# Kernel optimization log

Hardware: AMD Instinct MI355X
Metric: run time of the kernel (lower is better)

The kernel has to match this reference:

```python
import jax, jax.numpy as jnp
import numpy as np

NUM_HEADS = 12


def setup_inputs() -> dict:
    key = jax.random.key(0)
    ks = jax.random.split(key, 6)
    B, H, W, C = 8, 32, 32, 768
    hd = C // NUM_HEADS
    n = lambda k, shp, sc: jax.random.normal(k, shp, dtype=jnp.float32) * sc
    return {
        "x": n(ks[0], (B, H, W, C), 1.0),
        "qkv_w": n(ks[1], (3 * C, C), 0.02),
        "qkv_b": jnp.zeros((3 * C,), jnp.float32),
        "proj_w": n(ks[2], (C, C), 0.02),
        "proj_b": jnp.zeros((C,), jnp.float32),
        "rel_pos_h": n(ks[3], (2 * H - 1, hd), 0.02),
        "rel_pos_w": n(ks[4], (2 * W - 1, hd), 0.02),
    }


def reference(x, qkv_w, qkv_b, proj_w, proj_b, rel_pos_h, rel_pos_w):
    B, H, W, C = x.shape
    nH = NUM_HEADS
    hd = C // nH
    scale = hd ** -0.5
    # qkv projection (torch Linear convention: y = x @ W.T + b)
    qkv = x.reshape(B, H * W, C) @ qkv_w.T + qkv_b              # (B, HW, 3C)
    qkv = qkv.reshape(B, H * W, 3, nH, hd).transpose(2, 0, 3, 1, 4)
    qkv = qkv.reshape(3, B * nH, H * W, hd)
    q, k, v = qkv[0], qkv[1], qkv[2]
    attn = jnp.einsum('bqd,bkd->bqk', q * scale, k)             # (B*nH, HW, HW)
    # decomposed relative position bias (q_size == k_size, so no interpolation)
    coords_h = jnp.arange(H)[:, None] - jnp.arange(H)[None, :] + (H - 1)
    coords_w = jnp.arange(W)[:, None] - jnp.arange(W)[None, :] + (W - 1)
    Rh = rel_pos_h[coords_h]                                    # (H, H, hd)
    Rw = rel_pos_w[coords_w]                                    # (W, W, hd)
    r_q = q.reshape(B * nH, H, W, hd)
    rel_h = jnp.einsum('bhwc,hkc->bhwk', r_q, Rh)               # (B*nH, H, W, H)
    rel_w = jnp.einsum('bhwc,wkc->bhwk', r_q, Rw)               # (B*nH, H, W, W)
    attn = (attn.reshape(B * nH, H, W, H, W)
            + rel_h[..., :, None] + rel_w[..., None, :]).reshape(B * nH, H * W, H * W)
    attn = jax.nn.softmax(attn, axis=-1)
    out = attn @ v                                              # (B*nH, HW, hd)
    out = out.reshape(B, nH, H, W, hd).transpose(0, 2, 3, 1, 4).reshape(B, H, W, C)
    return out @ proj_w.T + proj_b
```

## Files before the change

kernel.cpp:

```cpp
#include <hip/hip_runtime.h>

using u16 = unsigned short;
using u32 = unsigned int;
typedef __attribute__((ext_vector_type(8))) short bf16x8;
typedef __attribute__((ext_vector_type(4))) float f32x4;

__device__ __forceinline__ float bf2f(u32 h) {
  union { u32 u; float f; } c; c.u = h << 16; return c.f;
}
__device__ __forceinline__ u16 f2bf(float f) {
  union { float f; u32 u; } c; c.f = f;
  u32 u = c.u;
  u32 r = (u + 0x7FFFu + ((u >> 16) & 1u)) >> 16;
  return (u16)r;
}

#define GLD16(gsrc, ldst)                                                      \
  __builtin_amdgcn_global_load_lds(                                            \
      (const __attribute__((address_space(1))) unsigned int*)(gsrc),           \
      (__attribute__((address_space(3))) unsigned int*)(ldst), 16, 0, 0)

__device__ __forceinline__ int kappa(int ss) {
  return (ss & 0x23) | ((ss & 0x10) >> 2) | ((ss & 0x0C) << 1);
}

__global__ void cvt_kernel(const float* __restrict__ src, u16* __restrict__ dst, int n) {
  int i = (blockIdx.x * blockDim.x + threadIdx.x) * 4;
  if (i < n) {
    float4 v = *(const float4*)(src + i);
    ushort4 o;
    o.x = f2bf(v.x); o.y = f2bf(v.y); o.z = f2bf(v.z); o.w = f2bf(v.w);
    *(ushort4*)(dst + i) = o;
  }
}

__global__ void tbl_kernel(const float* __restrict__ rph, const float* __restrict__ rpw,
                           u16* __restrict__ tbl) {
  int i = blockIdx.x * 256 + threadIdx.x;
  int row = i >> 6, d = i & 63;
  float v = 0.f;
  if (row < 63) v = rph[row * 64 + d];
  else if (row >= 64 && row < 127) v = rpw[(row - 64) * 64 + d];
  tbl[i] = f2bf(v * 8.0f);
}

__global__ void aug_kernel(u16* __restrict__ kb) {
  int j = blockIdx.x * 256 + threadIdx.x;
  int g = j >> 4, q4 = j & 15;
  int s = g & 1023;
  int d0 = 64 + q4 * 4;
  int kwslot = 64 + (s & 31);
  int khslot = 96 + (s >> 5);
  ushort4 v;
  v.x = (d0 == kwslot || d0 == khslot) ? 0x3F80 : 0;
  v.y = (d0 + 1 == kwslot || d0 + 1 == khslot) ? 0x3F80 : 0;
  v.z = (d0 + 2 == kwslot || d0 + 2 == khslot) ? 0x3F80 : 0;
  v.w = (d0 + 3 == kwslot || d0 + 3 == khslot) ? 0x3F80 : 0;
  *(ushort4*)&kb[(size_t)g * 128 + d0] = v;
}

__global__ __launch_bounds__(256, 2) void pgemm_kernel(
    const u16* __restrict__ A, const u16* __restrict__ tbl, u16* __restrict__ Q2) {
  __shared__ u16 As[128 * 64];
  __shared__ u16 Bs[128 * 64];
  const int tid = threadIdx.x;
  const int lane = tid & 63, wave = tid >> 6;
  const int lr = lane & 15, lg = lane >> 4;
  const int m0 = blockIdx.x * 128;
  const int wm = (wave >> 1) * 64, wn = (wave & 1) * 64;

#pragma unroll
  for (int i = 0; i < 4; ++i) {
    int c = tid + i * 256;
    int row = c >> 3, pp = c & 7;
    int pl = pp ^ (row & 7);
    GLD16(A + (size_t)(m0 + row) * 128 + pl * 8, &As[c * 8]);
    GLD16(tbl + row * 64 + pl * 8, &Bs[c * 8]);
  }
  __syncthreads();

  bf16x8 a[4][2], b[4][2];
#pragma unroll
  for (int m = 0; m < 4; ++m) {
    int row = wm + m * 16 + lr;
#pragma unroll
    for (int kf = 0; kf < 2; ++kf)
      a[m][kf] = *(const bf16x8*)&As[(row * 64 + kf * 32 + lg * 8) ^ ((row & 7) << 3)];
  }
#pragma unroll
  for (int n = 0; n < 4; ++n) {
    int row = wn + n * 16 + lr;
#pragma unroll
    for (int kf = 0; kf < 2; ++kf)
      b[n][kf] = *(const bf16x8*)&Bs[(row * 64 + kf * 32 + lg * 8) ^ ((row & 7) << 3)];
  }

  f32x4 acc[4][4] = {};
#pragma unroll
  for (int kf = 0; kf < 2; ++kf)
#pragma unroll
    for (int m = 0; m < 4; ++m)
#pragma unroll
      for (int n = 0; n < 4; ++n)
        acc[m][n] = __builtin_amdgcn_mfma_f32_16x16x32_bf16(a[m][kf], b[n][kf], acc[m][n], 0, 0, 0);

#pragma unroll
  for (int m = 0; m < 4; ++m)
#pragma unroll
    for (int n = 0; n < 4; ++n) {
      const int col = wn + n * 16 + lr;
#pragma unroll
      for (int r = 0; r < 4; ++r) {
        const int g = m0 + wm + m * 16 + lg * 4 + r;
        const int s = g & 1023;
        const int hq = s >> 5, w = s & 31;
        u16 hv = f2bf(acc[m][n][r]);
        if (col < 64) {
          int kh = hq + 31 - col;
          if ((unsigned)kh < 32u) Q2[(size_t)g * 128 + 96 + kh] = hv;
        } else {
          int kw = w + 95 - col;
          if ((unsigned)kw < 32u) Q2[(size_t)g * 128 + 64 + kw] = hv;
        }
      }
    }
}

template <int MODE>
__global__ __launch_bounds__(512, 2) void gemm128(
    const u16* __restrict__ A, const u16* __restrict__ B,
    const float* __restrict__ bias, u16* __restrict__ oq, u16* __restrict__ ok,
    u16* __restrict__ ovt, float* __restrict__ ofp) {
  __shared__ u16 As[2][128 * 64];
  __shared__ u16 Bs[2][128 * 64];
  const int tid = threadIdx.x;
  const int lane = tid & 63, wave = tid >> 6;
  const int lr = lane & 15, lg = lane >> 4;

  const int nbx = (MODE == 0) ? 18 : 6;
  const int nwg = nbx * 64;
  int id = blockIdx.y * nbx + blockIdx.x;
  int nid = (id & 7) * (nwg >> 3) + (id >> 3);
  const int m0 = (nid / nbx) * 128, n0 = (nid % nbx) * 128;
  const int wm = (wave >> 2) * 64, wn = (wave & 3) * 32;

  f32x4 acc[4][2] = {};

  const u16* ap[2];
  const u16* bp[2];
#pragma unroll
  for (int i = 0; i < 2; ++i) {
    int c = tid + i * 512;
    int row = c >> 3, pp = c & 7;
    int pl = pp ^ (row & 7);
    if constexpr (MODE == 0) {
      ap[i] = A + (size_t)(m0 + row) * 768 + pl * 8;
    } else {
      int g = m0 + row;
      ap[i] = A + ((size_t)((g >> 10) * 12) << 16) + (g & 1023) * 64 + pl * 8;
    }
    bp[i] = B + (size_t)(n0 + row) * 768 + pl * 8;
  }
  constexpr int dA = (MODE == 0) ? 64 : 65536;

  auto stage = [&](int bi) {
#pragma unroll
    for (int i = 0; i < 2; ++i) {
      int c = tid + i * 512;
      GLD16(ap[i], &As[bi][c * 8]);
      GLD16(bp[i], &Bs[bi][c * 8]);
      ap[i] += dA;
      bp[i] += 64;
    }
  };

  stage(0);
#pragma unroll 1
  for (int t = 0; t < 12; ++t) {
    const int cur = t & 1;
    if (t < 11) {
      stage(cur ^ 1);
      asm volatile("s_waitcnt vmcnt(4)" ::: "memory");
    } else {
      asm volatile("s_waitcnt vmcnt(0)" ::: "memory");
    }
    __builtin_amdgcn_sched_barrier(0);
    __builtin_amdgcn_s_barrier();
    __builtin_amdgcn_sched_barrier(0);

    bf16x8 a[4][2], b[2][2];
#pragma unroll
    for (int m = 0; m < 4; ++m) {
      int row = wm + m * 16 + lr;
#pragma unroll
      for (int kf = 0; kf < 2; ++kf)
        a[m][kf] = *(const bf16x8*)&As[cur][(row * 64 + kf * 32 + lg * 8) ^ ((row & 7) << 3)];
    }
#pragma unroll
    for (int n = 0; n < 2; ++n) {
      int row = wn + n * 16 + lr;
#pragma unroll
      for (int kf = 0; kf < 2; ++kf)
        b[n][kf] = *(const bf16x8*)&Bs[cur][(row * 64 + kf * 32 + lg * 8) ^ ((row & 7) << 3)];
    }
    __builtin_amdgcn_s_setprio(1);
#pragma unroll
    for (int kf = 0; kf < 2; ++kf)
#pragma unroll
      for (int m = 0; m < 4; ++m)
#pragma unroll
        for (int n = 0; n < 2; ++n)
          acc[m][n] = __builtin_amdgcn_mfma_f32_16x16x32_bf16(a[m][kf], b[n][kf], acc[m][n], 0, 0, 0);
    __builtin_amdgcn_s_setprio(0);

    __builtin_amdgcn_sched_barrier(0);
    __builtin_amdgcn_s_barrier();
    __builtin_amdgcn_sched_barrier(0);
  }

#pragma unroll
  for (int m = 0; m < 4; ++m) {
    const int grow0 = m0 + wm + m * 16 + lg * 4;
#pragma unroll
    for (int n = 0; n < 2; ++n) {
      const int gcol = n0 + wn + n * 16 + lr;
      const float bv = bias[gcol];
      if constexpr (MODE == 0) {
        int which = (gcol >= 1536) ? 2 : (gcol >= 768 ? 1 : 0);
        int rem = gcol - which * 768;
        int bh = (grow0 >> 10) * 12 + (rem >> 6);
        if (which == 2) {
          int s0 = grow0 & 1023;
          int colb = (s0 & ~63) | kappa(s0 & 63);
          ushort4 pk;
          pk.x = f2bf(acc[m][n][0] + bv);
          pk.y = f2bf(acc[m][n][1] + bv);
          pk.z = f2bf(acc[m][n][2] + bv);
          pk.w = f2bf(acc[m][n][3] + bv);
          *(ushort4*)&ovt[((size_t)bh << 16) + (size_t)(rem & 63) * 1024 + colb] = pk;
        } else {
          u16* dst = (which == 0) ? oq : ok;
          const float sc = (which == 0) ? 0.18033688f : 1.0f;
#pragma unroll
          for (int r = 0; r < 4; ++r) {
            int s = (grow0 & 1023) + r;
            dst[((size_t)bh << 17) + s * 128 + (rem & 63)] = f2bf((acc[m][n][r] + bv) * sc);
          }
        }
      } else {
#pragma unroll
        for (int r = 0; r < 4; ++r)
          ofp[(size_t)(grow0 + r) * 768 + gcol] = acc[m][n][r] + bv;
      }
    }
  }
}

__global__ __launch_bounds__(256, 2) void attn_kernel(
    const u16* __restrict__ qb, const u16* __restrict__ kb,
    const u16* __restrict__ vtb, u16* __restrict__ ao) {
  __shared__ u16 Ks[2][8192];
  __shared__ u16 Vs[2][4096];

  const int tid = threadIdx.x;
  const int lane = tid & 63, wave = tid >> 6;
  const int lr = lane & 15, lg = lane >> 4;
  const int bh = blockIdx.x;
  const int q0 = blockIdx.y * 128 + wave * 32;
  const size_t hb2 = (size_t)bh << 17;
  const size_t hbv = (size_t)bh << 16;

  bf16x8 qf[2][4];
#pragma unroll
  for (int m = 0; m < 2; ++m)
#pragma unroll
    for (int kf = 0; kf < 4; ++kf)
      qf[m][kf] = *(const bf16x8*)(qb + hb2 + (size_t)(q0 + m * 16 + lr) * 128 + kf * 32 + lg * 8);

  float lsum[2] = {};
  f32x4 acco[2][4] = {};

  const u16* kp[4];
  const u16* vp[2];
#pragma unroll
  for (int i = 0; i < 4; ++i) {
    int c = tid + i * 256;
    int half = c >> 9, row = (c >> 3) & 63, pp = c & 7;
    int pl = pp ^ (row & 7);
    kp[i] = kb + hb2 + (size_t)row * 128 + half * 64 + pl * 8;
  }
#pragma unroll
  for (int i = 0; i < 2; ++i) {
    int c = tid + i * 256;
    int row = c >> 3, pp = c & 7;
    int pl = pp ^ (row & 7);
    vp[i] = vtb + hbv + (size_t)row * 1024 + pl * 8;
  }

  auto stage = [&](int bi) {
#pragma unroll
    for (int i = 0; i < 4; ++i) {
      int c = tid + i * 256;
      GLD16(kp[i], &Ks[bi][c * 8]);
      kp[i] += 8192;
    }
#pragma unroll
    for (int i = 0; i < 2; ++i) {
      int c = tid + i * 256;
      GLD16(vp[i], &Vs[bi][c * 8]);
      vp[i] += 64;
    }
  };

  stage(0);

#pragma unroll 1
  for (int t = 0; t < 16; ++t) {
    const int cur = t & 1;
    if (t < 15) {
      stage(cur ^ 1);
      asm volatile("s_waitcnt vmcnt(6)" ::: "memory");
    } else {
      asm volatile("s_waitcnt vmcnt(0)" ::: "memory");
    }
    __builtin_amdgcn_sched_barrier(0);
    __builtin_amdgcn_s_barrier();
    __builtin_amdgcn_sched_barrier(0);

    f32x4 sac[2][4] = {};
    __builtin_amdgcn_s_setprio(1);
#pragma unroll
    for (int kf = 0; kf < 4; ++kf) {
      const int half = kf >> 1, kfl = kf & 1;
#pragma unroll
      for (int f = 0; f < 4; ++f) {
        int row = f * 16 + lr;
        bf16x8 kv = *(const bf16x8*)&Ks[cur][half * 4096 +
            ((row * 64 + kfl * 32 + lg * 8) ^ ((row & 7) << 3))];
#pragma unroll
        for (int m = 0; m < 2; ++m)
          sac[m][f] = __builtin_amdgcn_mfma_f32_16x16x32_bf16(kv, qf[m][kf], sac[m][f], 0, 0, 0);
      }
    }
    __builtin_amdgcn_s_setprio(0);

    bf16x8 paf[2][2];
#pragma unroll
    for (int m = 0; m < 2; ++m) {
      union { u32 w[4]; bf16x8 v; } wa, wb;
#pragma unroll
      for (int f = 0; f < 4; ++f) {
        float p0 = __builtin_amdgcn_exp2f(sac[m][f][0]);
        float p1 = __builtin_amdgcn_exp2f(sac[m][f][1]);
        float p2 = __builtin_amdgcn_exp2f(sac[m][f][2]);
        float p3 = __builtin_amdgcn_exp2f(sac[m][f][3]);
        lsum[m] += (p0 + p1) + (p2 + p3);
        u32 w0, w1;
        asm("v_cvt_pk_bf16_f32 %0, %1, %2" : "=v"(w0) : "v"(p0), "v"(p1));
        asm("v_cvt_pk_bf16_f32 %0, %1, %2" : "=v"(w1) : "v"(p2), "v"(p3));
        if (f < 2) { wa.w[f * 2] = w0; wa.w[f * 2 + 1] = w1; }
        else       { wb.w[(f - 2) * 2] = w0; wb.w[(f - 2) * 2 + 1] = w1; }
      }
      paf[m][0] = wa.v;
      paf[m][1] = wb.v;
    }

    __builtin_amdgcn_s_setprio(1);
#pragma unroll
    for (int kf = 0; kf < 2; ++kf) {
#pragma unroll
      for (int fd = 0; fd < 4; ++fd) {
        int drow = fd * 16 + lr;
        bf16x8 vv = *(const bf16x8*)&Vs[cur][(drow * 64 + kf * 32 + lg * 8) ^ ((drow & 7) << 3)];
#pragma unroll
        for (int m = 0; m < 2; ++m)
          acco[m][fd] = __builtin_amdgcn_mfma_f32_16x16x32_bf16(paf[m][kf], vv, acco[m][fd], 0, 0, 0);
      }
    }
    __builtin_amdgcn_s_setprio(0);

    __builtin_amdgcn_sched_barrier(0);
    __builtin_amdgcn_s_barrier();
    __builtin_amdgcn_sched_barrier(0);
  }

#pragma unroll
  for (int m = 0; m < 2; ++m) {
    float s = lsum[m];
    s += __shfl_xor(s, 16);
    s += __shfl_xor(s, 32);
    float inv = 1.0f / s;
#pragma unroll
    for (int r = 0; r < 4; ++r) {
      int src = (lane & 48) + ((lane & 48) >> 2) + r;
      float invr = __shfl(inv, src);
      int gq = q0 + m * 16 + lg * 4 + r;
#pragma unroll
      for (int fd = 0; fd < 4; ++fd)
        ao[hbv + (size_t)gq * 64 + fd * 16 + lr] = f2bf(acco[m][fd][r] * invr);
    }
  }
}

extern "C" void kernel_launch(void* const* d_in, const int* in_sizes, int n_in,
                              void* d_out, int out_size, void* d_ws, size_t ws_size,
                              hipStream_t stream) {
  const float* x = (const float*)d_in[0];
  const float* qkv_w = (const float*)d_in[1];
  const float* qkv_b = (const float*)d_in[2];
  const float* proj_w = (const float*)d_in[3];
  const float* proj_b = (const float*)d_in[4];
  const float* rel_pos_h = (const float*)d_in[5];
  const float* rel_pos_w = (const float*)d_in[6];
  float* out = (float*)d_out;

  char* ws = (char*)d_ws;
  u16* x_bf = (u16*)(ws + 0);
  u16* qkvw_bf = (u16*)(ws + 12582912);
  u16* projw_bf = (u16*)(ws + 16121856);
  u16* qbuf2 = (u16*)(ws + 17301504);
  u16* kbuf2 = (u16*)(ws + 42467328);
  u16* vtbuf = (u16*)(ws + 67633152);
  u16* tbl = (u16*)(ws + 80216064);
  u16* aobuf = x_bf;

  cvt_kernel<<<6144, 256, 0, stream>>>(x, x_bf, 6291456);
  cvt_kernel<<<1728, 256, 0, stream>>>(qkv_w, qkvw_bf, 1769472);
  cvt_kernel<<<576, 256, 0, stream>>>(proj_w, projw_bf, 589824);
  tbl_kernel<<<32, 256, 0, stream>>>(rel_pos_h, rel_pos_w, tbl);
  aug_kernel<<<6144, 256, 0, stream>>>(kbuf2);

  gemm128<0><<<dim3(18, 64), 512, 0, stream>>>(x_bf, qkvw_bf, qkv_b, qbuf2, kbuf2, vtbuf, nullptr);

  pgemm_kernel<<<768, 256, 0, stream>>>(qbuf2, tbl, qbuf2);

  attn_kernel<<<dim3(96, 8), 256, 0, stream>>>(qbuf2, kbuf2, vtbuf, aobuf);

  gemm128<1><<<dim3(6, 64), 512, 0, stream>>>(aobuf, projw_bf, proj_b, nullptr, nullptr, nullptr, out);
}
```

Before: 130.5 us.

## Generate relative-position one-hot K columns in registers instead of loading augmented K

The augmented K buffer, which stored one-hot columns for the relative-position bias, is replaced by a compact 64-wide K buffer. The one-hot key fragments are synthesised in registers inside the attention kernel (fixed width part, per-tile height part). This removes the aug_kernel launch, halves K global traffic and K LDS staging, and frees shared memory. In exchange the inner loop does some extra ALU work to build the fragments, while the MFMA count stays the same.

```diff
diff --git a/kernel.cpp b/kernel.cpp
--- a/kernel.cpp
+++ b/kernel.cpp
@@ -22,6 +22,14 @@
 
 __device__ __forceinline__ int kappa(int ss) {
   return (ss & 0x23) | ((ss & 0x10) >> 2) | ((ss & 0x0C) << 1);
+}
+
+__device__ __forceinline__ bf16x8 onehot8(int c) {
+  union { u32 w[4]; bf16x8 v; } u;
+  u32 hv = (c & 1) ? 0x3F800000u : 0x3F80u;
+#pragma unroll
+  for (int k = 0; k < 4; ++k) u.w[k] = ((c >> 1) == k) ? hv : 0u;
+  return u.v;
 }
 
 __global__ void cvt_kernel(const float* __restrict__ src, u16* __restrict__ dst, int n) {
@@ -42,21 +50,6 @@
   if (row < 63) v = rph[row * 64 + d];
   else if (row >= 64 && row < 127) v = rpw[(row - 64) * 64 + d];
   tbl[i] = f2bf(v * 8.0f);
-}
-
-__global__ void aug_kernel(u16* __restrict__ kb) {
-  int j = blockIdx.x * 256 + threadIdx.x;
-  int g = j >> 4, q4 = j & 15;
-  int s = g & 1023;
-  int d0 = 64 + q4 * 4;
-  int kwslot = 64 + (s & 31);
-  int khslot = 96 + (s >> 5);
-  ushort4 v;
-  v.x = (d0 == kwslot || d0 == khslot) ? 0x3F80 : 0;
-  v.y = (d0 + 1 == kwslot || d0 + 1 == khslot) ? 0x3F80 : 0;
-  v.z = (d0 + 2 == kwslot || d0 + 2 == khslot) ? 0x3F80 : 0;
-  v.w = (d0 + 3 == kwslot || d0 + 3 == khslot) ? 0x3F80 : 0;
-  *(ushort4*)&kb[(size_t)g * 128 + d0] = v;
 }
 
 __global__ __launch_bounds__(256, 2) void pgemm_kernel(
@@ -238,13 +231,18 @@
           pk.z = f2bf(acc[m][n][2] + bv);
           pk.w = f2bf(acc[m][n][3] + bv);
           *(ushort4*)&ovt[((size_t)bh << 16) + (size_t)(rem & 63) * 1024 + colb] = pk;
-        } else {
-          u16* dst = (which == 0) ? oq : ok;
-          const float sc = (which == 0) ? 0.18033688f : 1.0f;
+        } else if (which == 0) {
 #pragma unroll
           for (int r = 0; r < 4; ++r) {
             int s = (grow0 & 1023) + r;
-            dst[((size_t)bh << 17) + s * 128 + (rem & 63)] = f2bf((acc[m][n][r] + bv) * sc);
+            oq[((size_t)bh << 17) + s * 128 + (rem & 63)] =
+                f2bf((acc[m][n][r] + bv) * 0.18033688f);
+          }
+        } else {
+#pragma unroll
+          for (int r = 0; r < 4; ++r) {
+            int s = (grow0 & 1023) + r;
+            ok[((size_t)bh << 16) + s * 64 + (rem & 63)] = f2bf(acc[m][n][r] + bv);
           }
         }
       } else {
@@ -259,7 +257,7 @@
 __global__ __launch_bounds__(256, 2) void attn_kernel(
     const u16* __restrict__ qb, const u16* __restrict__ kb,
     const u16* __restrict__ vtb, u16* __restrict__ ao) {
-  __shared__ u16 Ks[2][8192];
+  __shared__ u16 Ks[2][4096];
   __shared__ u16 Vs[2][4096];
 
   const int tid = threadIdx.x;
@@ -277,37 +275,31 @@
     for (int kf = 0; kf < 4; ++kf)
       qf[m][kf] = *(const bf16x8*)(qb + hb2 + (size_t)(q0 + m * 16 + lr) * 128 + kf * 32 + lg * 8);
 
+  bf16x8 kwf[2];
+#pragma unroll
+  for (int h = 0; h < 2; ++h) kwf[h] = onehot8(h * 16 + lr - lg * 8);
+
   float lsum[2] = {};
   f32x4 acco[2][4] = {};
 
-  const u16* kp[4];
+  const u16* kp[2];
   const u16* vp[2];
-#pragma unroll
-  for (int i = 0; i < 4; ++i) {
-    int c = tid + i * 256;
-    int half = c >> 9, row = (c >> 3) & 63, pp = c & 7;
-    int pl = pp ^ (row & 7);
-    kp[i] = kb + hb2 + (size_t)row * 128 + half * 64 + pl * 8;
-  }
 #pragma unroll
   for (int i = 0; i < 2; ++i) {
     int c = tid + i * 256;
     int row = c >> 3, pp = c & 7;
     int pl = pp ^ (row & 7);
+    kp[i] = kb + hbv + (size_t)row * 64 + pl * 8;
     vp[i] = vtb + hbv + (size_t)row * 1024 + pl * 8;
   }
 
   auto stage = [&](int bi) {
 #pragma unroll
-    for (int i = 0; i < 4; ++i) {
+    for (int i = 0; i < 2; ++i) {
       int c = tid + i * 256;
       GLD16(kp[i], &Ks[bi][c * 8]);
-      kp[i] += 8192;
-    }
-#pragma unroll
-    for (int i = 0; i < 2; ++i) {
-      int c = tid + i * 256;
       GLD16(vp[i], &Vs[bi][c * 8]);
+      kp[i] += 4096;
       vp[i] += 64;
     }
   };
@@ -319,7 +311,7 @@
     const int cur = t & 1;
     if (t < 15) {
       stage(cur ^ 1);
-      asm volatile("s_waitcnt vmcnt(6)" ::: "memory");
+      asm volatile("s_waitcnt vmcnt(4)" ::: "memory");
     } else {
       asm volatile("s_waitcnt vmcnt(0)" ::: "memory");
     }
@@ -327,21 +319,33 @@
     __builtin_amdgcn_s_barrier();
     __builtin_amdgcn_sched_barrier(0);
 
+    bf16x8 khf[2];
+#pragma unroll
+    for (int h = 0; h < 2; ++h) khf[h] = onehot8(2 * t + h - lg * 8);
+
     f32x4 sac[2][4] = {};
     __builtin_amdgcn_s_setprio(1);
 #pragma unroll
-    for (int kf = 0; kf < 4; ++kf) {
-      const int half = kf >> 1, kfl = kf & 1;
+    for (int kf = 0; kf < 2; ++kf) {
 #pragma unroll
       for (int f = 0; f < 4; ++f) {
         int row = f * 16 + lr;
-        bf16x8 kv = *(const bf16x8*)&Ks[cur][half * 4096 +
-            ((row * 64 + kfl * 32 + lg * 8) ^ ((row & 7) << 3))];
+        bf16x8 kv = *(const bf16x8*)&Ks[cur][(row * 64 + kf * 32 + lg * 8) ^ ((row & 7) << 3)];
 #pragma unroll
         for (int m = 0; m < 2; ++m)
           sac[m][f] = __builtin_amdgcn_mfma_f32_16x16x32_bf16(kv, qf[m][kf], sac[m][f], 0, 0, 0);
       }
     }
+#pragma unroll
+    for (int f = 0; f < 4; ++f)
+#pragma unroll
+      for (int m = 0; m < 2; ++m)
+        sac[m][f] = __builtin_amdgcn_mfma_f32_16x16x32_bf16(kwf[f & 1], qf[m][2], sac[m][f], 0, 0, 0);
+#pragma unroll
+    for (int f = 0; f < 4; ++f)
+#pragma unroll
+      for (int m = 0; m < 2; ++m)
+        sac[m][f] = __builtin_amdgcn_mfma_f32_16x16x32_bf16(khf[f >> 1], qf[m][3], sac[m][f], 0, 0, 0);
     __builtin_amdgcn_s_setprio(0);
 
     bf16x8 paf[2][2];
@@ -419,22 +423,21 @@
   u16* qkvw_bf = (u16*)(ws + 12582912);
   u16* projw_bf = (u16*)(ws + 16121856);
   u16* qbuf2 = (u16*)(ws + 17301504);
-  u16* kbuf2 = (u16*)(ws + 42467328);
-  u16* vtbuf = (u16*)(ws + 67633152);
-  u16* tbl = (u16*)(ws + 80216064);
+  u16* kbuf = (u16*)(ws + 42467328);
+  u16* vtbuf = (u16*)(ws + 55050240);
+  u16* tbl = (u16*)(ws + 67633152);
   u16* aobuf = x_bf;
 
   cvt_kernel<<<6144, 256, 0, stream>>>(x, x_bf, 6291456);
   cvt_kernel<<<1728, 256, 0, stream>>>(qkv_w, qkvw_bf, 1769472);
   cvt_kernel<<<576, 256, 0, stream>>>(proj_w, projw_bf, 589824);
   tbl_kernel<<<32, 256, 0, stream>>>(rel_pos_h, rel_pos_w, tbl);
-  aug_kernel<<<6144, 256, 0, stream>>>(kbuf2);
-
-  gemm128<0><<<dim3(18, 64), 512, 0, stream>>>(x_bf, qkvw_bf, qkv_b, qbuf2, kbuf2, vtbuf, nullptr);
+
+  gemm128<0><<<dim3(18, 64), 512, 0, stream>>>(x_bf, qkvw_bf, qkv_b, qbuf2, kbuf, vtbuf, nullptr);
 
   pgemm_kernel<<<768, 256, 0, stream>>>(qbuf2, tbl, qbuf2);
 
-  attn_kernel<<<dim3(96, 8), 256, 0, stream>>>(qbuf2, kbuf2, vtbuf, aobuf);
+  attn_kernel<<<dim3(96, 8), 256, 0, stream>>>(qbuf2, kbuf, vtbuf, aobuf);
 
   gemm128<1><<<dim3(6, 64), 512, 0, stream>>>(aobuf, projw_bf, proj_b, nullptr, nullptr, nullptr, out);
 }
```

Result: faster. 124.6 us (-4.5%).
